# Kernel tuning notes

Hardware: AMD Instinct MI355X
Metric: run time of the kernel (lower is better)

The kernel has to match this reference:

```python
import jax, jax.numpy as jnp
import numpy as np

MARGIN = 1.0
N, D = 4096, 512
NUM_CLASSES = 64


def setup_inputs() -> dict:
    key = jax.random.key(0)
    k1, k2 = jax.random.split(key)
    inputs = jax.random.normal(k1, (N, D), dtype=jnp.float32)
    targets = jax.random.randint(k2, (N,), 0, NUM_CLASSES, dtype=jnp.int64)
    return {"inputs": inputs, "targets": targets}


def reference(inputs, targets):
    n = inputs.shape[0]
    sq = jnp.sum(inputs * inputs, axis=1)  # [n]
    # squared Euclidean distances, clamped at 0 (matches relu in original)
    d2 = jnp.maximum(sq[:, None] + sq[None, :] - 2.0 * (inputs @ inputs.T), 0.0)
    # safe sqrt (zero entries get 0, matching forward; avoids NaN grads)
    dist = jnp.where(d2 > 0, jnp.sqrt(jnp.where(d2 > 0, d2, 1.0)), 0.0)  # [n,n]

    same = targets[:, None] == targets[None, :]
    eye = jnp.eye(n, dtype=bool)
    pos_mask = same & ~eye          # positives, diagonal excluded
    neg_mask = ~same                # negatives (diagonal is same-label, excluded)

    # per-row sum_k exp(margin - d_ik) over negatives  (replaces per-pair loop)
    neg_sum = jnp.sum(jnp.where(neg_mask, jnp.exp(MARGIN - dist), 0.0), axis=1)  # [n]

    # J_ij = log(neg_sum_i + neg_sum_j) + d_ij for positive pairs
    J = jnp.log(neg_sum[:, None] + neg_sum[None, :]) + dist
    triu_pos = jnp.triu(pos_mask)   # loop iterated over upper-triangular positives
    hinge2 = jnp.where(triu_pos, jax.nn.relu(J) ** 2, 0.0)

    # original divides by count of ALL positive entries (both triangles)
    len_p = jnp.sum(pos_mask).astype(jnp.float32)
    return jnp.sum(hinge2) / len_p
```

## Files before the change

kernel.cpp:

```cpp
#include <hip/hip_runtime.h>
#include <math.h>

#define NN 4096
#define DD 512
#define MARGINF 1.0f
#define NCLS 64
#define MAXM 160
#define TRI (MAXM * (MAXM - 1) / 2)
#define PBLK 32
#define NBLK2 (PBLK * (PBLK + 1) / 2)
#define NSLICE 4

typedef __attribute__((ext_vector_type(8))) short bf16x8;
typedef __attribute__((ext_vector_type(4))) float f32x4;

#define WS_SQ   0
#define WS_NS   4096
#define WS_LOSS 8192
#define WS_CTR  8193
#define WS_LENP 8194
#define WS_RK   8320
#define WS_MEM  12416
#define WS_XF   32768
#define WS_PD   1081344

__device__ __forceinline__ unsigned short f2bf(float f) {
    unsigned u = __float_as_uint(f);
    u += 0x7fffu + ((u >> 16) & 1u);
    return (unsigned short)(u >> 16);
}

__global__ __launch_bounds__(256) void prep_kernel(const float* __restrict__ X,
                                                   const int* __restrict__ tgt,
                                                   float* __restrict__ ws) {
    __shared__ int tg[NN];
    const int tid = threadIdx.x;
    for (int j = tid; j < NN; j += 256) tg[j] = tgt[j];

    const int wv = tid >> 6, lane = tid & 63;
    const int row = blockIdx.x * 4 + wv;
    const float4* xr = (const float4*)(X + (size_t)row * DD);
    float4 a = xr[2 * lane], b = xr[2 * lane + 1];
    float s = a.x * a.x + a.y * a.y + a.z * a.z + a.w * a.w
            + b.x * b.x + b.y * b.y + b.z * b.z + b.w * b.w;
#pragma unroll
    for (int off = 32; off; off >>= 1) s += __shfl_down(s, off, 64);

    ushort4 pa = {f2bf(a.x), f2bf(a.y), f2bf(a.z), f2bf(a.w)};
    ushort4 pb = {f2bf(b.x), f2bf(b.y), f2bf(b.z), f2bf(b.w)};
    const int r16 = row >> 4, m = row & 15;
    const int kb = lane >> 2, q = lane & 3;
    ushort4* dst = (ushort4*)((unsigned short*)(ws + WS_XF)
                              + ((size_t)(r16 * 16 + kb) * 64 + q * 16 + m) * 8);
    dst[0] = pa;
    dst[1] = pb;

    __syncthreads();
    const int myc = tg[row];
    int cnt = 0;
    for (int j = lane; j < row; j += 64) cnt += (tg[j] == myc) ? 1 : 0;
#pragma unroll
    for (int off = 32; off; off >>= 1) cnt += __shfl_down(cnt, off, 64);
    if (lane == 0) {
        ws[WS_SQ + row] = s;
        ws[WS_NS + row] = 0.0f;
        ((int*)(ws + WS_RK))[row] = cnt;
        if (cnt < MAXM) ((int*)(ws + WS_MEM))[myc * MAXM + cnt] = row;
    }
    if (blockIdx.x == 0 && tid == 0) {
        ws[WS_LOSS] = 0.0f;
        ((unsigned*)ws)[WS_CTR] = 0u;
        ws[WS_LENP] = 0.0f;
    }
}

__device__ __forceinline__ void stage8(const unsigned short* __restrict__ gpanel,
                                       int t, int fbase, int lane,
                                       unsigned short* lbase) {
#pragma unroll
    for (int s = 0; s < 8; ++s) {
        const int fi = fbase + s;
        const unsigned short* gp =
            gpanel + ((size_t)((fi >> 1) * 16 + t * 2 + (fi & 1))) * 512 + lane * 8;
        __builtin_amdgcn_global_load_lds(
            (const __attribute__((address_space(1))) int*)gp,
            (__attribute__((address_space(3))) int*)(lbase + fi * 512),
            16, 0, 0);
    }
}

__global__ __launch_bounds__(256, 2) void negsum_kernel(const int* __restrict__ tgt,
                                                        float* __restrict__ ws) {
    __shared__ unsigned short lds[2][2][16][512];
    const int bidx = blockIdx.x;
    int bj = (int)((sqrtf(8.0f * (float)bidx + 1.0f) - 1.0f) * 0.5f);
    while (bj * (bj + 1) / 2 > bidx) --bj;
    while ((bj + 1) * (bj + 2) / 2 <= bidx) ++bj;
    const int bi = bidx - bj * (bj + 1) / 2;
    const int i0 = bi * 128, j0 = bj * 128;

    const int tid = threadIdx.x;
    const int w = tid >> 6, lane = tid & 63;
    const int m_ = lane & 15, q = lane >> 4;
    const int wr = (w & 1) * 64, wc = (w >> 1) * 64;
    const unsigned short* Xf = (const unsigned short*)(ws + WS_XF);

    const int ab = w >> 1;
    const int fbase = (w & 1) * 8;
    const unsigned short* gpanel = Xf + (size_t)(ab ? bj : bi) * 8 * 8192;
    unsigned short* lb0 = &lds[0][ab][0][0];
    unsigned short* lb1 = &lds[1][ab][0][0];

    f32x4 acc[4][4] = {};

    stage8(gpanel, 0, fbase, lane, lb0);
    __syncthreads();
#pragma unroll 2
    for (int t = 0; t < 8; ++t) {
        const int cur = t & 1;
        if (t < 7) stage8(gpanel, t + 1, fbase, lane, cur ? lb0 : lb1);
#pragma unroll
        for (int kbl = 0; kbl < 2; ++kbl) {
            bf16x8 af[4], bf[4];
#pragma unroll
            for (int u = 0; u < 4; ++u)
                af[u] = *(const bf16x8*)&lds[cur][0][((w & 1) * 4 + u) * 2 + kbl][lane * 8];
#pragma unroll
            for (int v = 0; v < 4; ++v)
                bf[v] = *(const bf16x8*)&lds[cur][1][((w >> 1) * 4 + v) * 2 + kbl][lane * 8];
#pragma unroll
            for (int u = 0; u < 4; ++u)
#pragma unroll
                for (int v = 0; v < 4; ++v)
                    acc[u][v] = __builtin_amdgcn_mfma_f32_16x16x32_bf16(
                        af[u], bf[v], acc[u][v], 0, 0, 0);
        }
        __syncthreads();
    }

    const float* sq = ws + WS_SQ;
    float* ns = ws + WS_NS;
    const int* rk = (const int*)(ws + WS_RK);
    float* posd = ws + WS_PD;
    float sjv[4]; int tjv[4], jv[4];
#pragma unroll
    for (int v = 0; v < 4; ++v) {
        int j = j0 + wc + v * 16 + m_;
        jv[v] = j;
        sjv[v] = sq[j];
        tjv[v] = tgt[j];
    }
    float colp[4] = {0.0f, 0.0f, 0.0f, 0.0f};
#pragma unroll
    for (int u = 0; u < 4; ++u) {
#pragma unroll
        for (int r = 0; r < 4; ++r) {
            const int i = i0 + wr + u * 16 + q * 4 + r;
            const float si = sq[i];
            const int ti = tgt[i];
            float rp = 0.0f;
#pragma unroll
            for (int v = 0; v < 4; ++v) {
                float d2 = si + sjv[v] - 2.0f * acc[u][v][r];
                float dist = d2 > 0.0f ? sqrtf(d2) : 0.0f;
                if (tjv[v] != ti) {
                    float e = __expf(MARGINF - dist);
                    rp += e;
                    colp[v] += e;
                } else if (i < jv[v]) {
                    int ra = rk[i], rb = rk[jv[v]];
                    if (ra < MAXM && rb < MAXM) {
                        int hi = ra > rb ? ra : rb;
                        int lo = ra > rb ? rb : ra;
                        posd[ti * TRI + hi * (hi - 1) / 2 + lo] = dist;
                    }
                }
            }
            rp += __shfl_xor(rp, 1, 64);
            rp += __shfl_xor(rp, 2, 64);
            rp += __shfl_xor(rp, 4, 64);
            rp += __shfl_xor(rp, 8, 64);
            if (m_ == 0) atomicAdd(&ns[i], rp);
        }
    }
    if (bi != bj) {
#pragma unroll
        for (int v = 0; v < 4; ++v) {
            float cp = colp[v];
            cp += __shfl_xor(cp, 16, 64);
            cp += __shfl_xor(cp, 32, 64);
            if (q == 0) atomicAdd(&ns[jv[v]], cp);
        }
    }
}

__global__ __launch_bounds__(256) void pair2_kernel(const int* __restrict__ tgt,
                                                    float* __restrict__ ws,
                                                    float* __restrict__ out) {
    __shared__ float wsum[4];
    __shared__ int csum[4];
    __shared__ bool last;
    const int c = blockIdx.x >> 2;
    const int sl = blockIdx.x & 3;
    const int tid = threadIdx.x;
    const int wv = tid >> 6, lane = tid & 63;

    int ccount = 0;
    for (int j = tid; j < NN; j += 256) ccount += (tgt[j] == c) ? 1 : 0;
#pragma unroll
    for (int off = 32; off; off >>= 1) ccount += __shfl_down(ccount, off, 64);
    if (lane == 0) csum[wv] = ccount;
    __syncthreads();
    int mc = csum[0] + csum[1] + csum[2] + csum[3];
    if (mc > MAXM) mc = MAXM;
    const int P = mc * (mc - 1) / 2;

    const int* mem = (const int*)(ws + WS_MEM) + c * MAXM;
    const float* pd = ws + WS_PD + c * TRI;
    const float* ns = ws + WS_NS;
    float lsum = 0.0f;
    for (int p = tid + sl * 256; p < P; p += 256 * NSLICE) {
        int b = (int)((1.0f + sqrtf(1.0f + 8.0f * (float)p)) * 0.5f);
        while (b * (b - 1) / 2 > p) --b;
        while ((b + 1) * b / 2 <= p) ++b;
        const int a = p - b * (b - 1) / 2;
        const float dist = pd[b * (b - 1) / 2 + a];
        const int i = mem[a], j = mem[b];
        float J = __logf(ns[i] + ns[j]) + dist;
        float h = fmaxf(J, 0.0f);
        lsum += h * h;
    }
#pragma unroll
    for (int off = 32; off; off >>= 1) lsum += __shfl_xor(lsum, off, 64);
    if (lane == 0) wsum[wv] = lsum;
    __syncthreads();
    if (tid == 0) {
        float s = wsum[0] + wsum[1] + wsum[2] + wsum[3];
        if (s != 0.0f) atomicAdd(&ws[WS_LOSS], s);
        if (sl == 0) atomicAdd(&ws[WS_LENP], (float)(mc * (mc - 1)));
        __threadfence();
        unsigned d = atomicAdd((unsigned*)ws + WS_CTR, 1u);
        last = (d == NCLS * NSLICE - 1);
    }
    __syncthreads();
    if (last && tid == 0) {
        float total = atomicAdd(&ws[WS_LOSS], 0.0f);
        float lp = atomicAdd(&ws[WS_LENP], 0.0f);
        out[0] = total / lp;
    }
}

extern "C" void kernel_launch(void* const* d_in, const int* in_sizes, int n_in,
                              void* d_out, int out_size, void* d_ws, size_t ws_size,
                              hipStream_t stream) {
    const float* X  = (const float*)d_in[0];
    const int*  tgt = (const int*)d_in[1];
    float* ws  = (float*)d_ws;
    float* out = (float*)d_out;

    hipLaunchKernelGGL(prep_kernel, dim3(NN / 4), dim3(256), 0, stream, X, tgt, ws);
    hipLaunchKernelGGL(negsum_kernel, dim3(NBLK2), dim3(256), 0, stream, tgt, ws);
    hipLaunchKernelGGL(pair2_kernel, dim3(NCLS * NSLICE), dim3(256), 0, stream, tgt, ws, out);
}
```

Baseline: 134.7 us.

## Load MFMA fragments directly from global into registers, drop LDS staging

Removes the LDS double-buffered staging via global_load_lds and has each wave load its bf16 fragments straight from global memory into a register double buffer across the full K loop, eliminating __syncthreads. Raises launch-bounds occupancy to 3 blocks per CU and remaps block indices with a stride-66 swizzle, likely to spread tiles across XCDs for L2 locality. The cost is that A/B panels are no longer shared through LDS, so each wave issues redundant global loads and relies on caches to absorb the reuse.

```diff
diff --git a/kernel.cpp b/kernel.cpp
--- a/kernel.cpp
+++ b/kernel.cpp
@@ -74,25 +74,9 @@
     }
 }
 
-__device__ __forceinline__ void stage8(const unsigned short* __restrict__ gpanel,
-                                       int t, int fbase, int lane,
-                                       unsigned short* lbase) {
-#pragma unroll
-    for (int s = 0; s < 8; ++s) {
-        const int fi = fbase + s;
-        const unsigned short* gp =
-            gpanel + ((size_t)((fi >> 1) * 16 + t * 2 + (fi & 1))) * 512 + lane * 8;
-        __builtin_amdgcn_global_load_lds(
-            (const __attribute__((address_space(1))) int*)gp,
-            (__attribute__((address_space(3))) int*)(lbase + fi * 512),
-            16, 0, 0);
-    }
-}
-
-__global__ __launch_bounds__(256, 2) void negsum_kernel(const int* __restrict__ tgt,
+__global__ __launch_bounds__(256, 3) void negsum_kernel(const int* __restrict__ tgt,
                                                         float* __restrict__ ws) {
-    __shared__ unsigned short lds[2][2][16][512];
-    const int bidx = blockIdx.x;
+    const int bidx = (blockIdx.x & 7) * 66 + (blockIdx.x >> 3);
     int bj = (int)((sqrtf(8.0f * (float)bidx + 1.0f) - 1.0f) * 0.5f);
     while (bj * (bj + 1) / 2 > bidx) --bj;
     while ((bj + 1) * (bj + 2) / 2 <= bidx) ++bj;
@@ -105,37 +89,32 @@
     const int wr = (w & 1) * 64, wc = (w >> 1) * 64;
     const unsigned short* Xf = (const unsigned short*)(ws + WS_XF);
 
-    const int ab = w >> 1;
-    const int fbase = (w & 1) * 8;
-    const unsigned short* gpanel = Xf + (size_t)(ab ? bj : bi) * 8 * 8192;
-    unsigned short* lb0 = &lds[0][ab][0][0];
-    unsigned short* lb1 = &lds[1][ab][0][0];
+    const unsigned short* pA = Xf + (size_t)((i0 + wr) >> 4) * 8192 + lane * 8;
+    const unsigned short* pB = Xf + (size_t)((j0 + wc) >> 4) * 8192 + lane * 8;
 
     f32x4 acc[4][4] = {};
-
-    stage8(gpanel, 0, fbase, lane, lb0);
-    __syncthreads();
-#pragma unroll 2
-    for (int t = 0; t < 8; ++t) {
-        const int cur = t & 1;
-        if (t < 7) stage8(gpanel, t + 1, fbase, lane, cur ? lb0 : lb1);
-#pragma unroll
-        for (int kbl = 0; kbl < 2; ++kbl) {
-            bf16x8 af[4], bf[4];
-#pragma unroll
-            for (int u = 0; u < 4; ++u)
-                af[u] = *(const bf16x8*)&lds[cur][0][((w & 1) * 4 + u) * 2 + kbl][lane * 8];
+    bf16x8 bufA[2][4], bufB[2][4];
+#pragma unroll
+    for (int u = 0; u < 4; ++u) {
+        bufA[0][u] = *(const bf16x8*)(pA + u * 8192);
+        bufB[0][u] = *(const bf16x8*)(pB + u * 8192);
+    }
+#pragma unroll
+    for (int t = 0; t < 16; ++t) {
+        const int cur = t & 1, nx = cur ^ 1;
+        if (t < 15) {
+#pragma unroll
+            for (int u = 0; u < 4; ++u) {
+                bufA[nx][u] = *(const bf16x8*)(pA + u * 8192 + (t + 1) * 512);
+                bufB[nx][u] = *(const bf16x8*)(pB + u * 8192 + (t + 1) * 512);
+            }
+        }
+#pragma unroll
+        for (int u = 0; u < 4; ++u)
 #pragma unroll
             for (int v = 0; v < 4; ++v)
-                bf[v] = *(const bf16x8*)&lds[cur][1][((w >> 1) * 4 + v) * 2 + kbl][lane * 8];
-#pragma unroll
-            for (int u = 0; u < 4; ++u)
-#pragma unroll
-                for (int v = 0; v < 4; ++v)
-                    acc[u][v] = __builtin_amdgcn_mfma_f32_16x16x32_bf16(
-                        af[u], bf[v], acc[u][v], 0, 0, 0);
-        }
-        __syncthreads();
+                acc[u][v] = __builtin_amdgcn_mfma_f32_16x16x32_bf16(
+                    bufA[cur][u], bufB[cur][v], acc[u][v], 0, 0, 0);
     }
 
     const float* sq = ws + WS_SQ;
```

New measurement: 122.4 us. 1.1x faster.
